# Optimization experiments

Measured on AMD Instinct MI355X. Metric: run time of the kernel, lower is better.

Reference implementation:

```python
import jax, jax.numpy as jnp
import numpy as np
from jax import lax

SCORE_T = 0.05
NMS_T = 0.5
MAXDET = 300


def batch_iou(b1, b2):
    # b1: [K,4], b2: [K,4] -> [K,K]
    lt = jnp.maximum(b1[:, None, :2], b2[None, :, :2])
    rb = jnp.minimum(b1[:, None, 2:], b2[None, :, 2:])
    inter = jnp.clip(rb - lt, 0.0, None).prod(-1)
    a1 = (b1[:, 2:] - b1[:, :2]).prod(-1)
    a2 = (b2[:, 2:] - b2[:, :2]).prod(-1)
    union = a1[:, None] + a2[None, :] - inter
    return inter / jnp.clip(union, 1e-7, None)


def nms_class(boxes, cls_scores):
    # boxes: [N,4], cls_scores: [N]. Mirrors: score>thresh filter, top-k MAXDET
    # candidates, greedy NMS in descending score order.
    s = jnp.where(cls_scores > SCORE_T, cls_scores, -jnp.inf)
    top_s, idx = lax.top_k(s, MAXDET)          # sorted desc, [K]
    b = jnp.take(boxes, idx, axis=0)            # [K,4]
    v = jnp.isfinite(top_s)                     # passed score threshold
    iou = batch_iou(b, b)                       # [K,K]

    def body(kept, i):
        # keep i iff valid and no already-kept box has IoU >= NMS_T with it
        suppressed = jnp.any(jnp.where(kept, iou[i], 0.0) >= NMS_T)
        return kept.at[i].set(v[i] & ~suppressed), None

    kept, _ = lax.scan(body, jnp.zeros(MAXDET, dtype=bool), jnp.arange(MAXDET))
    return top_s, idx, kept


def per_image(boxes, cls):
    # boxes: [N,4], cls: [N,C]
    C = cls.shape[1]
    top_s, idx, kept = jax.vmap(nms_class, in_axes=(None, 1))(boxes, cls)  # [C,K]
    scores_flat = jnp.where(kept, top_s, -jnp.inf).reshape(-1)  # [C*K]
    idx_flat = idx.reshape(-1)
    labels_flat = jnp.repeat(jnp.arange(C), MAXDET)
    fs, fi = lax.top_k(scores_flat, MAXDET)     # global top-k across classes
    valid = jnp.isfinite(fs)
    box_idx = idx_flat[fi]
    out_boxes = jnp.where(valid[:, None], jnp.take(boxes, box_idx, axis=0), -1.0)
    out_scores = jnp.where(valid, fs, -1.0)
    out_labels = jnp.where(valid, labels_flat[fi], -1).astype(jnp.int32)
    return out_boxes, out_scores, out_labels


def setup_inputs() -> dict:
    key = jax.random.key(0)
    k1, k2, k3 = jax.random.split(key, 3)
    B, N, C = 8, 100000, 80
    centers = jax.random.uniform(k1, (B, N, 2), dtype=jnp.float32) * 1024.0
    wh = jax.random.uniform(k2, (B, N, 2), dtype=jnp.float32) * 96.0 + 4.0
    boxes = jnp.concatenate([centers - wh / 2, centers + wh / 2], axis=-1)
    classification = jax.random.uniform(k3, (B, N, C), dtype=jnp.float32)
    return {"boxes": boxes, "classification": classification}


def reference(boxes, classification):
    # Returns (Boxes [B,MAXDET,4], Scores [B,MAXDET], Labels [B,MAXDET] int32),
    # padded with -1 where fewer than MAXDET detections survive.
    return jax.vmap(per_image)(boxes, classification)
```

## Files before the change

### kernel.cpp

```cpp
#include <hip/hip_runtime.h>

#define BIMG 8
#define NBOX 100000
#define NCLS 80
#define KDET 300
#define CAP  2048
#define CAPC 20
#define TPUSH 0.984375f
#define SCORE_T 0.05f
#define NELEM 8000000
#define NQ    2000000

typedef unsigned long long u64;
typedef unsigned u32;

#define OFF_PUSHCNT 0u
#define ZERO_BYTES  2560u
#define OFF_BUF     4096u
#define OFF_KCNT    (4096u + 10485760u)
#define OFF_KSC     (OFF_KCNT + 2560u)
#define OFF_KIDX    (OFF_KSC + 768000u)

static __device__ __forceinline__ u64 mk_key(float sc, u32 n) {
  return ((u64)__float_as_uint(sc) << 32) | (u32)(~n);
}

static __device__ __forceinline__ void radix_step(const u32* hist, int nbins,
                                                  int width, u32* sk, u64* spfx,
                                                  u32* stot) {
  if (threadIdx.x < 64) {
    const int lane = threadIdx.x;
    const int chunk = nbins >> 6;
    u32 psum = 0;
    for (int i = 0; i < chunk; ++i) psum += hist[lane * chunk + i];
    u32 suf = psum;
#pragma unroll
    for (int off = 1; off < 64; off <<= 1) {
      u32 o = __shfl_down(suf, off);
      if (lane + off < 64) suf += o;
    }
    if (lane == 0) *stot = suf;
    u32 k = *sk;
    u64 bal = __ballot(suf >= k);
    if (bal != 0ull) {
      int L = 63 - __clzll((long long)bal);
      if (lane == L) {
        u32 krem = k - (suf - psum);
        int bi = (L + 1) * chunk - 1;
        u32 acc = 0;
        for (;;) {
          acc += hist[bi];
          if (acc >= krem || bi == L * chunk) break;
          --bi;
        }
        *spfx = (*spfx << width) | (u32)bi;
        *sk = krem - (acc - hist[bi]);
      }
    }
  }
}

__constant__ int RSH[6] = {53, 42, 31, 20, 9, 0};
__constant__ int RWD[6] = {11, 11, 11, 11, 11, 9};

static __device__ __forceinline__ void pushone(int c, float sc, u32 n, int b,
                                               u32* lcnt, u64* stage,
                                               u32* pushcnt, u64* buf) {
  u64 key = mk_key(sc, n);
  u32 slot = atomicAdd(&lcnt[c], 1u);
  if (slot < CAPC) {
    stage[c * CAPC + slot] = key;
  } else {
    u32 g = atomicAdd(&pushcnt[b * NCLS + c], 1u);
    if (g < CAP) buf[(size_t)(b * NCLS + c) * CAP + g] = key;
  }
}

__global__ __launch_bounds__(256) void histK(const float* __restrict__ cls,
                                             u32* __restrict__ pushcnt,
                                             u64* __restrict__ buf) {
  __shared__ u32 lcnt[NCLS];
  __shared__ u32 sbase[NCLS];
  __shared__ u64 stage[NCLS * CAPC];

  const int t = threadIdx.x;
  const int b = blockIdx.y;
  for (int i = t; i < NCLS; i += 256) lcnt[i] = 0;
  __syncthreads();

  const float4* base4 = (const float4*)(cls + (size_t)b * NELEM);
  const int start = blockIdx.x * 8192;

#define LOADQ(u) const int q##u = qb + (u) * 256; \
  const float4 v##u = (q##u < NQ) ? base4[q##u] : make_float4(0.f, 0.f, 0.f, 0.f)
#define PROCQ(u) do { \
    float mx = fmaxf(fmaxf(v##u.x, v##u.y), fmaxf(v##u.z, v##u.w)); \
    if (mx >= TPUSH) { \
      const int e0 = q##u * 4; \
      const int c0 = e0 % NCLS; \
      const u32 n = (u32)(e0 / NCLS); \
      if (v##u.x >= TPUSH) pushone(c0 + 0, v##u.x, n, b, lcnt, stage, pushcnt, buf); \
      if (v##u.y >= TPUSH) pushone(c0 + 1, v##u.y, n, b, lcnt, stage, pushcnt, buf); \
      if (v##u.z >= TPUSH) pushone(c0 + 2, v##u.z, n, b, lcnt, stage, pushcnt, buf); \
      if (v##u.w >= TPUSH) pushone(c0 + 3, v##u.w, n, b, lcnt, stage, pushcnt, buf); \
    } } while (0)

  for (int it = 0; it < 4; ++it) {
    const int qb = start + it * 2048 + t;
    LOADQ(0); LOADQ(1); LOADQ(2); LOADQ(3);
    LOADQ(4); LOADQ(5); LOADQ(6); LOADQ(7);
    PROCQ(0); PROCQ(1); PROCQ(2); PROCQ(3);
    PROCQ(4); PROCQ(5); PROCQ(6); PROCQ(7);
  }
#undef LOADQ
#undef PROCQ
  __syncthreads();

  if (t < NCLS) {
    u32 cnt = min(lcnt[t], (u32)CAPC);
    sbase[t] = cnt ? atomicAdd(&pushcnt[b * NCLS + t], cnt) : 0u;
  }
  __syncthreads();
  for (int idx = t; idx < NCLS * CAPC; idx += 256) {
    const int c = idx / CAPC;
    const int k = idx - c * CAPC;
    if ((u32)k < min(lcnt[c], (u32)CAPC)) {
      u32 s = sbase[c] + (u32)k;
      if (s < CAP) buf[(size_t)(b * NCLS + c) * CAP + s] = stage[idx];
    }
  }
}

__global__ __launch_bounds__(256) void fbK(const float* __restrict__ cls,
                                           u32* __restrict__ pushcnt,
                                           u64* __restrict__ buf) {
  const int bc = blockIdx.x;
  const u32 cnt = pushcnt[bc];
  if (cnt >= KDET && cnt <= CAP) return;

  __shared__ u32 hist[2048];
  __shared__ u32 sprefix, sk, sabove, seq, stot, smode;

  const int t = threadIdx.x;
  const int b = bc / NCLS, c = bc % NCLS;
  const float* col = cls + (size_t)b * NELEM + c;
  if (t == 0) { atomicExch(&pushcnt[bc], 0u); smode = 0; }

  for (int r = 0; r < 3; ++r) {
    const int shift = (r == 0) ? 21 : (r == 1) ? 10 : 0;
    const int nbins = (r == 2) ? 1024 : 2048;
    for (int i = t; i < nbins; i += 256) hist[i] = 0;
    __syncthreads();
    for (int n = t; n < NBOX; n += 256) {
      float sc = col[(size_t)n * NCLS];
      if (sc > SCORE_T) {
        u32 u = __float_as_uint(sc);
        bool ok = (r == 0) || (r == 1 ? ((u >> 21) == (sprefix >> 21))
                                      : ((u >> 10) == (sprefix >> 10)));
        if (ok) atomicAdd(&hist[(u >> shift) & (u32)(nbins - 1)], 1u);
      }
    }
    __syncthreads();
    if (t == 0) {
      if (r == 0) {
        u32 s = 0;
        for (int i = 0; i < nbins; ++i) s += hist[i];
        stot = s;
        if (s < KDET) smode = 1;
      }
      if (smode == 0) {
        u32 kk = (r == 0) ? (u32)KDET : sk;
        u32 acc = 0;
        int bi = nbins - 1;
        for (; bi >= 0; --bi) {
          if (acc + hist[bi] >= kk) break;
          acc += hist[bi];
        }
        sk = kk - acc;
        sprefix = ((r == 0) ? 0u : sprefix) | ((u32)bi << shift);
        if (r == 2) { seq = hist[bi]; sabove = KDET - sk; }
      }
    }
    __syncthreads();
    if (smode == 1) break;
  }

  if (smode == 1) {
    for (int n = t; n < NBOX; n += 256) {
      float sc = col[(size_t)n * NCLS];
      if (sc > SCORE_T) {
        u32 g = atomicAdd(&pushcnt[bc], 1u);
        if (g < CAP) buf[(size_t)bc * CAP + g] = mk_key(sc, (u32)n);
      }
    }
    return;
  }

  const u32 ustar = sprefix;
  const u32 m = sabove, e = seq;
  if (m + e <= CAP) {
    for (int n = t; n < NBOX; n += 256) {
      float sc = col[(size_t)n * NCLS];
      if (sc > SCORE_T && __float_as_uint(sc) >= ustar) {
        u32 g = atomicAdd(&pushcnt[bc], 1u);
        if (g < CAP) buf[(size_t)bc * CAP + g] = mk_key(sc, (u32)n);
      }
    }
  } else {
    for (int n = t; n < NBOX; n += 256) {
      float sc = col[(size_t)n * NCLS];
      if (sc > SCORE_T && __float_as_uint(sc) > ustar) {
        u32 g = atomicAdd(&pushcnt[bc], 1u);
        if (g < CAP) buf[(size_t)bc * CAP + g] = mk_key(sc, (u32)n);
      }
    }
    __syncthreads();
    if (t == 0) {
      u32 room = CAP - m, got = 0;
      for (int n = 0; n < NBOX && got < room; ++n) {
        float sc = col[(size_t)n * NCLS];
        if (sc > SCORE_T && __float_as_uint(sc) == ustar) {
          u32 g = atomicAdd(&pushcnt[bc], 1u);
          if (g < CAP) buf[(size_t)bc * CAP + g] = mk_key(sc, (u32)n);
          ++got;
        }
      }
    }
  }
}

__global__ __launch_bounds__(512) void nmsK(const float* __restrict__ boxes,
                                            const u32* __restrict__ pushcnt,
                                            const u64* __restrict__ buf,
                                            u32* __restrict__ keptCnt,
                                            float* __restrict__ keptScore,
                                            u32* __restrict__ keptIdx) {
  __shared__ float bx[KDET][4];
  __shared__ float scl[KDET];
  __shared__ u32 nn_[KDET];
  __shared__ u64 msk[KDET][5];
  __shared__ u64 tk[512];
  __shared__ u64 anyw[5];
  __shared__ u64 keptw[5];
  __shared__ u64 spfx;
  __shared__ u32 sk, stot, stcnt;

  const int t = threadIdx.x;
  const int bc = blockIdx.x;
  const int b = bc / NCLS;
  const int cnt = min((int)pushcnt[bc], CAP);
  const u64* src = buf + (size_t)bc * CAP;

  u64 kk[4];
#pragma unroll
  for (int u = 0; u < 4; ++u) {
    int i = t + u * 512;
    kk[u] = (i < cnt) ? src[i] : 0ull;
  }
  if (t == 0) { spfx = 0ull; sk = KDET; stcnt = 0u; }
  if (t < 5) anyw[t] = 0ull;
  u32* hist = (u32*)&msk[0][0];

  const bool normal = (cnt > KDET);
  if (normal) {
    for (int p = 0; p < 6; ++p) {
      const int nb = (p == 5) ? 512 : 2048;
      for (int i = t; i < nb; i += 512) hist[i] = 0;
      __syncthreads();
      const u64 pfx = spfx;
#pragma unroll
      for (int u = 0; u < 4; ++u) {
        u64 key = kk[u];
        if (!key) continue;
        if (p > 0 && (key >> RSH[p - 1]) != pfx) continue;
        atomicAdd(&hist[(u32)(key >> RSH[p]) & (u32)(nb - 1)], 1u);
      }
      __syncthreads();
      radix_step(hist, nb, RWD[p], &sk, &spfx, &stot);
      __syncthreads();
    }
  } else {
    __syncthreads();
  }
  const u64 thr = normal ? spfx : 1ull;

  tk[t] = 0ull;
  __syncthreads();
#pragma unroll
  for (int u = 0; u < 4; ++u) {
    u64 key = kk[u];
    if (key >= thr && key != 0ull) {
      u32 pos = atomicAdd(&stcnt, 1u);
      if (pos < 512) tk[pos] = key;
    }
  }
  __syncthreads();

  for (int k2 = 2; k2 <= 512; k2 <<= 1) {
    for (int j = k2 >> 1; j > 0; j >>= 1) {
      int i = t, ixj = i ^ j;
      if (ixj > i) {
        u64 a = tk[i], c2 = tk[ixj];
        bool up = ((i & k2) == 0);
        if (up ? (a < c2) : (a > c2)) { tk[i] = c2; tk[ixj] = a; }
      }
      __syncthreads();
    }
  }

  const int M = min((int)stcnt, KDET);
  for (int i = t; i < M; i += 512) {
    u64 key = tk[i];
    u32 n = ~(u32)key;
    scl[i] = __uint_as_float((u32)(key >> 32));
    nn_[i] = n;
    const float4 bv = *(const float4*)(boxes + ((size_t)b * NBOX + n) * 4);
    bx[i][0] = bv.x; bx[i][1] = bv.y; bx[i][2] = bv.z; bx[i][3] = bv.w;
  }
  __syncthreads();

  for (int i = t; i < M; i += 512) {
    float x1 = bx[i][0], y1 = bx[i][1], x2 = bx[i][2], y2 = bx[i][3];
    float a1 = (x2 - x1) * (y2 - y1);
    u64 m0 = 0, m1 = 0, m2 = 0, m3 = 0, m4 = 0;
    for (int j = 0; j < i; ++j) {
      float lx = fmaxf(x1, bx[j][0]);
      float ly = fmaxf(y1, bx[j][1]);
      float rx = fminf(x2, bx[j][2]);
      float ry = fminf(y2, bx[j][3]);
      float iw = fmaxf(rx - lx, 0.0f), ih = fmaxf(ry - ly, 0.0f);
      float inter = iw * ih;
      float a2 = (bx[j][2] - bx[j][0]) * (bx[j][3] - bx[j][1]);
      float uni = fmaxf(a1 + a2 - inter, 1e-7f);
      float iou = inter / uni;
      if (iou >= 0.5f) {
        u64 bit = 1ull << (j & 63);
        switch (j >> 6) {
          case 0: m0 |= bit; break;
          case 1: m1 |= bit; break;
          case 2: m2 |= bit; break;
          case 3: m3 |= bit; break;
          default: m4 |= bit; break;
        }
      }
    }
    msk[i][0] = m0; msk[i][1] = m1; msk[i][2] = m2; msk[i][3] = m3; msk[i][4] = m4;
    if (m0 | m1 | m2 | m3 | m4) atomicOr(&anyw[i >> 6], 1ull << (i & 63));
  }
  __syncthreads();

  if (t == 0) {
    u64 kw[5] = {0, 0, 0, 0, 0};
    u64 aw[5] = {anyw[0], anyw[1], anyw[2], anyw[3], anyw[4]};
    for (int i = 0; i < M; ++i) {
      bool sup = false;
      if ((aw[i >> 6] >> (i & 63)) & 1ull) {
        u64 s0 = (msk[i][0] & kw[0]) | (msk[i][1] & kw[1]) |
                 (msk[i][2] & kw[2]) | (msk[i][3] & kw[3]) |
                 (msk[i][4] & kw[4]);
        sup = (s0 != 0ull);
      }
      if (!sup) kw[i >> 6] |= 1ull << (i & 63);
    }
    keptw[0] = kw[0]; keptw[1] = kw[1]; keptw[2] = kw[2];
    keptw[3] = kw[3]; keptw[4] = kw[4];
  }
  __syncthreads();

  for (int i = t; i < M; i += 512) {
    if ((keptw[i >> 6] >> (i & 63)) & 1ull) {
      int rank = 0;
      for (int w = 0; w < (i >> 6); ++w) rank += __popcll(keptw[w]);
      rank += __popcll(keptw[i >> 6] & ((1ull << (i & 63)) - 1ull));
      keptScore[(size_t)bc * KDET + rank] = scl[i];
      keptIdx[(size_t)bc * KDET + rank] = nn_[i];
    }
  }
  if (t == 0) {
    int tot = 0;
    for (int w = 0; w < 5; ++w) tot += __popcll(keptw[w]);
    keptCnt[bc] = (u32)tot;
  }
}

#define MSLOT 24
__global__ __launch_bounds__(1024) void mergeK(const float* __restrict__ boxes,
                                               const u32* __restrict__ keptCnt,
                                               const float* __restrict__ keptScore,
                                               const u32* __restrict__ keptIdx,
                                               float* __restrict__ out) {
  __shared__ u32 hist[4 * 2048];
  __shared__ int scnt[NCLS];
  __shared__ u64 tk[512];
  __shared__ u64 spfx, sthr;
  __shared__ u32 sk, stot, smode, stcnt;

  const int t = threadIdx.x;
  const int b = blockIdx.x;
  if (t < NCLS) scnt[t] = min((int)keptCnt[b * NCLS + t], KDET);
  if (t == 0) { spfx = 0ull; sk = KDET; smode = 0u; stcnt = 0u; }
  __syncthreads();

  u64 kk[MSLOT];
  const float* ksc = keptScore + (size_t)b * NCLS * KDET;
#pragma unroll
  for (int u = 0; u < MSLOT; ++u) {
    int idx = t + u * 1024;
    u64 key = 0ull;
    if (idx < NCLS * KDET) {
      int c = idx / KDET, r = idx - c * KDET;
      if (r < scnt[c])
        key = ((u64)__float_as_uint(ksc[idx]) << 32) | (u32)(~(u32)idx);
    }
    kk[u] = key;
  }

  for (int p = 0; p < 6; ++p) {
    const int nb = (p == 5) ? 512 : 2048;
    for (int i = t; i < 4 * 2048; i += 1024) hist[i] = 0;
    __syncthreads();
    u32* hp = hist + ((t >> 8) & 3) * 2048;
    const u64 pfx = spfx;
#pragma unroll
    for (int u = 0; u < MSLOT; ++u) {
      u64 key = kk[u];
      if (!key) continue;
      if (p > 0 && (key >> RSH[p - 1]) != pfx) continue;
      atomicAdd(&hp[(u32)(key >> RSH[p]) & (u32)(nb - 1)], 1u);
    }
    __syncthreads();
    for (int i = t; i < nb; i += 1024)
      hist[i] = hist[i] + hist[2048 + i] + hist[4096 + i] + hist[6144 + i];
    __syncthreads();
    radix_step(hist, nb, RWD[p], &sk, &spfx, &stot);
    __syncthreads();
    if (p == 0) {
      if (t == 0 && stot <= KDET) smode = 1u;
      __syncthreads();
      if (smode) break;
    }
  }
  if (t == 0) sthr = smode ? 1ull : spfx;
  if (t < 512) tk[t] = 0ull;
  __syncthreads();

  const u64 thr = sthr;
#pragma unroll
  for (int u = 0; u < MSLOT; ++u) {
    u64 key = kk[u];
    if (key >= thr && key != 0ull) {
      u32 pos = atomicAdd(&stcnt, 1u);
      if (pos < 512) tk[pos] = key;
    }
  }
  __syncthreads();

  for (int k2 = 2; k2 <= 512; k2 <<= 1) {
    for (int j = k2 >> 1; j > 0; j >>= 1) {
      if (t < 512) {
        int i = t, ixj = i ^ j;
        if (ixj > i) {
          u64 a = tk[i], c2 = tk[ixj];
          bool up = ((i & k2) == 0);
          if (up ? (a < c2) : (a > c2)) { tk[i] = c2; tk[ixj] = a; }
        }
      }
      __syncthreads();
    }
  }

  if (t < KDET) {
    float* ob = out + ((size_t)b * KDET + t) * 4;
    float* os = out + (size_t)BIMG * KDET * 4;
    float* ol = os + (size_t)BIMG * KDET;
    u64 key = tk[t];
    if (key == 0ull) {
      *(float4*)ob = make_float4(-1.f, -1.f, -1.f, -1.f);
      os[(size_t)b * KDET + t] = -1.f;
      ol[(size_t)b * KDET + t] = -1.f;
    } else {
      u32 fi = ~(u32)key;
      int c = fi / KDET, r = fi - c * KDET;
      u32 n = keptIdx[((size_t)b * NCLS + c) * KDET + r];
      *(float4*)ob = *(const float4*)(boxes + ((size_t)b * NBOX + n) * 4);
      os[(size_t)b * KDET + t] = __uint_as_float((u32)(key >> 32));
      ol[(size_t)b * KDET + t] = (float)c;
    }
  }
}

extern "C" void kernel_launch(void* const* d_in, const int* in_sizes, int n_in,
                              void* d_out, int out_size, void* d_ws, size_t ws_size,
                              hipStream_t stream) {
  const float* boxes = (const float*)d_in[0];
  const float* cls = (const float*)d_in[1];
  float* out = (float*)d_out;
  char* ws = (char*)d_ws;

  u32* pushcnt = (u32*)(ws + OFF_PUSHCNT);
  u64* buf = (u64*)(ws + OFF_BUF);
  u32* keptCnt = (u32*)(ws + OFF_KCNT);
  float* keptScore = (float*)(ws + OFF_KSC);
  u32* keptIdx = (u32*)(ws + OFF_KIDX);

  (void)hipMemsetAsync(ws + OFF_PUSHCNT, 0, ZERO_BYTES, stream);

  histK<<<dim3(246, BIMG), 256, 0, stream>>>(cls, pushcnt, buf);
  fbK<<<BIMG * NCLS, 256, 0, stream>>>(cls, pushcnt, buf);
  nmsK<<<BIMG * NCLS, 512, 0, stream>>>(boxes, pushcnt, buf, keptCnt, keptScore, keptIdx);
  mergeK<<<BIMG, 1024, 0, stream>>>(boxes, keptCnt, keptScore, keptIdx, out);
}
```

Before: 524.2 us.

## Fuse fallback selection into NMS kernel and parallelize sort and greedy suppression

Removes the separate fallback kernel: its radix-select and re-scan now run at the top of the NMS kernel, with a block-local shared counter instead of global atomics. The bitonic sort now uses wavefront shuffles for strides up to 32 instead of a block-wide barrier after every step. The single-thread greedy suppression loop becomes a 64-lane ballot-based pass over each 64-box word. The histogram kernel gets a bounds-check-free fast path for full tiles, and its grid drops the one extra empty block. The cost is a larger, more register-heavy NMS kernel in which the rare fallback path scans a strided column with 512 threads.

Measured after the change: 513.0 us. 1.02x faster.

```diff
diff --git a/kernel.cpp b/kernel.cpp
--- a/kernel.cpp
+++ b/kernel.cpp
@@ -91,8 +91,6 @@
   const float4* base4 = (const float4*)(cls + (size_t)b * NELEM);
   const int start = blockIdx.x * 8192;
 
-#define LOADQ(u) const int q##u = qb + (u) * 256; \
-  const float4 v##u = (q##u < NQ) ? base4[q##u] : make_float4(0.f, 0.f, 0.f, 0.f)
 #define PROCQ(u) do { \
     float mx = fmaxf(fmaxf(v##u.x, v##u.y), fmaxf(v##u.z, v##u.w)); \
     if (mx >= TPUSH) { \
@@ -105,14 +103,28 @@
       if (v##u.w >= TPUSH) pushone(c0 + 3, v##u.w, n, b, lcnt, stage, pushcnt, buf); \
     } } while (0)
 
-  for (int it = 0; it < 4; ++it) {
-    const int qb = start + it * 2048 + t;
-    LOADQ(0); LOADQ(1); LOADQ(2); LOADQ(3);
-    LOADQ(4); LOADQ(5); LOADQ(6); LOADQ(7);
-    PROCQ(0); PROCQ(1); PROCQ(2); PROCQ(3);
-    PROCQ(4); PROCQ(5); PROCQ(6); PROCQ(7);
-  }
-#undef LOADQ
+  if (start + 8192 <= NQ) {
+    for (int it = 0; it < 4; ++it) {
+      const int qb = start + it * 2048 + t;
+#define LOADF(u) const int q##u = qb + (u) * 256; const float4 v##u = base4[q##u]
+      LOADF(0); LOADF(1); LOADF(2); LOADF(3);
+      LOADF(4); LOADF(5); LOADF(6); LOADF(7);
+#undef LOADF
+      PROCQ(0); PROCQ(1); PROCQ(2); PROCQ(3);
+      PROCQ(4); PROCQ(5); PROCQ(6); PROCQ(7);
+    }
+  } else {
+    for (int it = 0; it < 4; ++it) {
+      const int qb = start + it * 2048 + t;
+#define LOADC(u) const int q##u = qb + (u) * 256; \
+  const float4 v##u = (q##u < NQ) ? base4[q##u] : make_float4(0.f, 0.f, 0.f, 0.f)
+      LOADC(0); LOADC(1); LOADC(2); LOADC(3);
+      LOADC(4); LOADC(5); LOADC(6); LOADC(7);
+#undef LOADC
+      PROCQ(0); PROCQ(1); PROCQ(2); PROCQ(3);
+      PROCQ(4); PROCQ(5); PROCQ(6); PROCQ(7);
+    }
+  }
 #undef PROCQ
   __syncthreads();
 
@@ -131,107 +143,10 @@
   }
 }
 
-__global__ __launch_bounds__(256) void fbK(const float* __restrict__ cls,
-                                           u32* __restrict__ pushcnt,
-                                           u64* __restrict__ buf) {
-  const int bc = blockIdx.x;
-  const u32 cnt = pushcnt[bc];
-  if (cnt >= KDET && cnt <= CAP) return;
-
-  __shared__ u32 hist[2048];
-  __shared__ u32 sprefix, sk, sabove, seq, stot, smode;
-
-  const int t = threadIdx.x;
-  const int b = bc / NCLS, c = bc % NCLS;
-  const float* col = cls + (size_t)b * NELEM + c;
-  if (t == 0) { atomicExch(&pushcnt[bc], 0u); smode = 0; }
-
-  for (int r = 0; r < 3; ++r) {
-    const int shift = (r == 0) ? 21 : (r == 1) ? 10 : 0;
-    const int nbins = (r == 2) ? 1024 : 2048;
-    for (int i = t; i < nbins; i += 256) hist[i] = 0;
-    __syncthreads();
-    for (int n = t; n < NBOX; n += 256) {
-      float sc = col[(size_t)n * NCLS];
-      if (sc > SCORE_T) {
-        u32 u = __float_as_uint(sc);
-        bool ok = (r == 0) || (r == 1 ? ((u >> 21) == (sprefix >> 21))
-                                      : ((u >> 10) == (sprefix >> 10)));
-        if (ok) atomicAdd(&hist[(u >> shift) & (u32)(nbins - 1)], 1u);
-      }
-    }
-    __syncthreads();
-    if (t == 0) {
-      if (r == 0) {
-        u32 s = 0;
-        for (int i = 0; i < nbins; ++i) s += hist[i];
-        stot = s;
-        if (s < KDET) smode = 1;
-      }
-      if (smode == 0) {
-        u32 kk = (r == 0) ? (u32)KDET : sk;
-        u32 acc = 0;
-        int bi = nbins - 1;
-        for (; bi >= 0; --bi) {
-          if (acc + hist[bi] >= kk) break;
-          acc += hist[bi];
-        }
-        sk = kk - acc;
-        sprefix = ((r == 0) ? 0u : sprefix) | ((u32)bi << shift);
-        if (r == 2) { seq = hist[bi]; sabove = KDET - sk; }
-      }
-    }
-    __syncthreads();
-    if (smode == 1) break;
-  }
-
-  if (smode == 1) {
-    for (int n = t; n < NBOX; n += 256) {
-      float sc = col[(size_t)n * NCLS];
-      if (sc > SCORE_T) {
-        u32 g = atomicAdd(&pushcnt[bc], 1u);
-        if (g < CAP) buf[(size_t)bc * CAP + g] = mk_key(sc, (u32)n);
-      }
-    }
-    return;
-  }
-
-  const u32 ustar = sprefix;
-  const u32 m = sabove, e = seq;
-  if (m + e <= CAP) {
-    for (int n = t; n < NBOX; n += 256) {
-      float sc = col[(size_t)n * NCLS];
-      if (sc > SCORE_T && __float_as_uint(sc) >= ustar) {
-        u32 g = atomicAdd(&pushcnt[bc], 1u);
-        if (g < CAP) buf[(size_t)bc * CAP + g] = mk_key(sc, (u32)n);
-      }
-    }
-  } else {
-    for (int n = t; n < NBOX; n += 256) {
-      float sc = col[(size_t)n * NCLS];
-      if (sc > SCORE_T && __float_as_uint(sc) > ustar) {
-        u32 g = atomicAdd(&pushcnt[bc], 1u);
-        if (g < CAP) buf[(size_t)bc * CAP + g] = mk_key(sc, (u32)n);
-      }
-    }
-    __syncthreads();
-    if (t == 0) {
-      u32 room = CAP - m, got = 0;
-      for (int n = 0; n < NBOX && got < room; ++n) {
-        float sc = col[(size_t)n * NCLS];
-        if (sc > SCORE_T && __float_as_uint(sc) == ustar) {
-          u32 g = atomicAdd(&pushcnt[bc], 1u);
-          if (g < CAP) buf[(size_t)bc * CAP + g] = mk_key(sc, (u32)n);
-          ++got;
-        }
-      }
-    }
-  }
-}
-
 __global__ __launch_bounds__(512) void nmsK(const float* __restrict__ boxes,
+                                            const float* __restrict__ cls,
                                             const u32* __restrict__ pushcnt,
-                                            const u64* __restrict__ buf,
+                                            u64* __restrict__ buf,
                                             u32* __restrict__ keptCnt,
                                             float* __restrict__ keptScore,
                                             u32* __restrict__ keptIdx) {
@@ -240,26 +155,118 @@
   __shared__ u32 nn_[KDET];
   __shared__ u64 msk[KDET][5];
   __shared__ u64 tk[512];
-  __shared__ u64 anyw[5];
   __shared__ u64 keptw[5];
   __shared__ u64 spfx;
   __shared__ u32 sk, stot, stcnt;
+  __shared__ u32 sfpfx, sfk, sfab, sfeq, sfmode, sfbcnt;
 
   const int t = threadIdx.x;
   const int bc = blockIdx.x;
   const int b = bc / NCLS;
-  const int cnt = min((int)pushcnt[bc], CAP);
-  const u64* src = buf + (size_t)bc * CAP;
+  u64* bufp = buf + (size_t)bc * CAP;
+  u32* hist = (u32*)&msk[0][0];
+
+  if (t == 0) { spfx = 0ull; sk = KDET; stcnt = 0u; sfmode = 0u; sfbcnt = 0u; }
+
+  u32 realcnt = pushcnt[bc];
+  const bool dofb = !(realcnt >= (u32)KDET && realcnt <= (u32)CAP);
+  if (dofb) {
+    const int c = bc % NCLS;
+    const float* col = cls + (size_t)b * NELEM + c;
+    for (int r = 0; r < 3; ++r) {
+      const int shift = (r == 0) ? 21 : (r == 1) ? 10 : 0;
+      const int nbins = (r == 2) ? 1024 : 2048;
+      for (int i = t; i < nbins; i += 512) hist[i] = 0;
+      __syncthreads();
+      for (int n = t; n < NBOX; n += 512) {
+        float sc = col[(size_t)n * NCLS];
+        if (sc > SCORE_T) {
+          u32 u = __float_as_uint(sc);
+          bool ok = (r == 0) || (r == 1 ? ((u >> 21) == (sfpfx >> 21))
+                                        : ((u >> 10) == (sfpfx >> 10)));
+          if (ok) atomicAdd(&hist[(u >> shift) & (u32)(nbins - 1)], 1u);
+        }
+      }
+      __syncthreads();
+      if (t == 0) {
+        if (r == 0) {
+          u32 s = 0;
+          for (int i = 0; i < nbins; ++i) s += hist[i];
+          if (s < KDET) sfmode = 1u;
+        }
+        if (sfmode == 0u) {
+          u32 kk2 = (r == 0) ? (u32)KDET : sfk;
+          u32 acc = 0;
+          int bi = nbins - 1;
+          for (; bi >= 0; --bi) {
+            if (acc + hist[bi] >= kk2) break;
+            acc += hist[bi];
+          }
+          sfk = kk2 - acc;
+          sfpfx = ((r == 0) ? 0u : sfpfx) | ((u32)bi << shift);
+          if (r == 2) { sfeq = hist[bi]; sfab = KDET - sfk; }
+        }
+      }
+      __syncthreads();
+      if (sfmode == 1u) break;
+    }
+
+    if (sfmode == 1u) {
+      for (int n = t; n < NBOX; n += 512) {
+        float sc = col[(size_t)n * NCLS];
+        if (sc > SCORE_T) {
+          u32 g = atomicAdd(&sfbcnt, 1u);
+          if (g < CAP) bufp[g] = mk_key(sc, (u32)n);
+        }
+      }
+    } else {
+      const u32 ustar = sfpfx;
+      const u32 m = sfab, e = sfeq;
+      if (m + e <= CAP) {
+        for (int n = t; n < NBOX; n += 512) {
+          float sc = col[(size_t)n * NCLS];
+          if (sc > SCORE_T && __float_as_uint(sc) >= ustar) {
+            u32 g = atomicAdd(&sfbcnt, 1u);
+            if (g < CAP) bufp[g] = mk_key(sc, (u32)n);
+          }
+        }
+      } else {
+        for (int n = t; n < NBOX; n += 512) {
+          float sc = col[(size_t)n * NCLS];
+          if (sc > SCORE_T && __float_as_uint(sc) > ustar) {
+            u32 g = atomicAdd(&sfbcnt, 1u);
+            if (g < CAP) bufp[g] = mk_key(sc, (u32)n);
+          }
+        }
+        __syncthreads();
+        if (t == 0) {
+          u32 room = CAP - m, got = 0;
+          for (int n = 0; n < NBOX && got < room; ++n) {
+            float sc = col[(size_t)n * NCLS];
+            if (sc > SCORE_T && __float_as_uint(sc) == ustar) {
+              u32 g = atomicAdd(&sfbcnt, 1u);
+              if (g < CAP) bufp[g] = mk_key(sc, (u32)n);
+              ++got;
+            }
+          }
+        }
+      }
+    }
+    __threadfence_block();
+    __syncthreads();
+    realcnt = sfbcnt;
+  }
+  const int cnt = min((int)realcnt, CAP);
 
   u64 kk[4];
 #pragma unroll
   for (int u = 0; u < 4; ++u) {
     int i = t + u * 512;
-    kk[u] = (i < cnt) ? src[i] : 0ull;
-  }
-  if (t == 0) { spfx = 0ull; sk = KDET; stcnt = 0u; }
-  if (t < 5) anyw[t] = 0ull;
-  u32* hist = (u32*)&msk[0][0];
+    u64 v = 0ull;
+    if (i < cnt)
+      v = dofb ? *((volatile const u64*)(bufp + i)) : bufp[i];
+    kk[u] = v;
+  }
 
   const bool normal = (cnt > KDET);
   if (normal) {
@@ -296,17 +303,41 @@
   }
   __syncthreads();
 
-  for (int k2 = 2; k2 <= 512; k2 <<= 1) {
+  u64 a = tk[t];
+#pragma unroll
+  for (int k2 = 2; k2 <= 64; k2 <<= 1) {
+#pragma unroll
     for (int j = k2 >> 1; j > 0; j >>= 1) {
-      int i = t, ixj = i ^ j;
-      if (ixj > i) {
-        u64 a = tk[i], c2 = tk[ixj];
-        bool up = ((i & k2) == 0);
-        if (up ? (a < c2) : (a > c2)) { tk[i] = c2; tk[ixj] = a; }
-      }
-      __syncthreads();
-    }
-  }
+      u64 c2 = __shfl_xor(a, j);
+      bool takeMax = (((t & k2) == 0) == ((t & j) == 0));
+      u64 mx = (a > c2) ? a : c2;
+      u64 mn = (a > c2) ? c2 : a;
+      a = takeMax ? mx : mn;
+    }
+  }
+#pragma unroll
+  for (int k2 = 128; k2 <= 512; k2 <<= 1) {
+    for (int j = k2 >> 1; j >= 64; j >>= 1) {
+      tk[t] = a;
+      __syncthreads();
+      u64 c2 = tk[t ^ j];
+      bool takeMax = (((t & k2) == 0) == ((t & j) == 0));
+      u64 mx = (a > c2) ? a : c2;
+      u64 mn = (a > c2) ? c2 : a;
+      a = takeMax ? mx : mn;
+      __syncthreads();
+    }
+#pragma unroll
+    for (int j = 32; j > 0; j >>= 1) {
+      u64 c2 = __shfl_xor(a, j);
+      bool takeMax = (((t & k2) == 0) == ((t & j) == 0));
+      u64 mx = (a > c2) ? a : c2;
+      u64 mn = (a > c2) ? c2 : a;
+      a = takeMax ? mx : mn;
+    }
+  }
+  tk[t] = a;
+  __syncthreads();
 
   const int M = min((int)stcnt, KDET);
   for (int i = t; i < M; i += 512) {
@@ -345,25 +376,33 @@
       }
     }
     msk[i][0] = m0; msk[i][1] = m1; msk[i][2] = m2; msk[i][3] = m3; msk[i][4] = m4;
-    if (m0 | m1 | m2 | m3 | m4) atomicOr(&anyw[i >> 6], 1ull << (i & 63));
-  }
-  __syncthreads();
-
-  if (t == 0) {
-    u64 kw[5] = {0, 0, 0, 0, 0};
-    u64 aw[5] = {anyw[0], anyw[1], anyw[2], anyw[3], anyw[4]};
-    for (int i = 0; i < M; ++i) {
-      bool sup = false;
-      if ((aw[i >> 6] >> (i & 63)) & 1ull) {
-        u64 s0 = (msk[i][0] & kw[0]) | (msk[i][1] & kw[1]) |
-                 (msk[i][2] & kw[2]) | (msk[i][3] & kw[3]) |
-                 (msk[i][4] & kw[4]);
-        sup = (s0 != 0ull);
-      }
-      if (!sup) kw[i >> 6] |= 1ull << (i & 63);
-    }
-    keptw[0] = kw[0]; keptw[1] = kw[1]; keptw[2] = kw[2];
-    keptw[3] = kw[3]; keptw[4] = kw[4];
+  }
+  __syncthreads();
+
+  if (t < 64) {
+    u64 kwv[5];
+#pragma unroll
+    for (int w = 0; w < 5; ++w) {
+      const int i = w * 64 + t;
+      bool pb = (i < M);
+      u64 mown = 0ull;
+      if (pb) {
+#pragma unroll
+        for (int w2 = 0; w2 < 5; ++w2)
+          if (w2 < w && (msk[i][w2] & kwv[w2])) pb = false;
+        mown = msk[i][w];
+      }
+      u64 kv = 0ull;
+      for (;;) {
+        u64 bal = __ballot(pb && ((mown & kv) == 0ull));
+        if (!bal) break;
+        int p = __ffsll((unsigned long long)bal) - 1;
+        kv |= 1ull << p;
+        if (t == p) pb = false;
+      }
+      kwv[w] = kv;
+      if (t == 0) keptw[w] = kv;
+    }
   }
   __syncthreads();
 
@@ -505,8 +544,8 @@
 
   (void)hipMemsetAsync(ws + OFF_PUSHCNT, 0, ZERO_BYTES, stream);
 
-  histK<<<dim3(246, BIMG), 256, 0, stream>>>(cls, pushcnt, buf);
-  fbK<<<BIMG * NCLS, 256, 0, stream>>>(cls, pushcnt, buf);
-  nmsK<<<BIMG * NCLS, 512, 0, stream>>>(boxes, pushcnt, buf, keptCnt, keptScore, keptIdx);
+  histK<<<dim3(245, BIMG), 256, 0, stream>>>(cls, pushcnt, buf);
+  nmsK<<<BIMG * NCLS, 512, 0, stream>>>(boxes, cls, pushcnt, buf, keptCnt,
+                                        keptScore, keptIdx);
   mergeK<<<BIMG, 1024, 0, stream>>>(boxes, keptCnt, keptScore, keptIdx, out);
 }
```
